# Kernel tuning notes

Hardware: AMD Instinct MI355X
Metric: run time of the kernel (lower is better)

Reference implementation:

```python
import jax, jax.numpy as jnp
import numpy as np

B = 16        # number of lists
N = 1024      # items per list (all equal)
D = 256       # feature dim (= dim_emb, need_embedding=False)


def setup_inputs() -> dict:
    key = jax.random.key(0)
    k1, k2, k3 = jax.random.split(key, 3)
    feats = jax.random.normal(k1, (B * N, D), dtype=jnp.float32)
    length = jnp.full((B,), N, dtype=jnp.int32)
    # Bilinear params: torch nn.Bilinear(d, d, 1) -> weight [1, d, d], bias [1]
    # xavier_uniform on the 3-d weight: bound = sqrt(6 / (fan_in + fan_out)) with
    # fan_in = d (last dim), fan_out = 1*d (per torch _calculate_fan_in_and_fan_out)
    bound = float(np.sqrt(6.0 / (D + D)))
    W_upper = jax.random.uniform(k2, (1, D, D), jnp.float32, -bound, bound)
    W_lower = jax.random.uniform(k3, (1, D, D), jnp.float32, -bound, bound)
    b_upper = jnp.zeros((1,), jnp.float32)
    b_lower = jnp.zeros((1,), jnp.float32)
    return {"feats": feats, "W_upper": W_upper, "b_upper": b_upper,
            "W_lower": W_lower, "b_lower": b_lower, "length": length}


def reference(feats, W_upper, b_upper, W_lower, b_lower, length):
    # nb_layers=0, need_embedding=False -> embedding and transformer are Identity.
    b = length.shape[0]
    n = feats.shape[0] // b  # equal-length lists -> static reshape
    d = feats.shape[-1]
    X = feats.reshape(b, n, d)  # [B, n, d]
    # For list i: repeated_feats_1 row (p*n + q) = x_p, repeated_feats_2 row = x_q,
    # so adjacency[p, q] = x_p^T W x_q + bias  (Bilinear with out=1).
    upper = jnp.einsum('bnd,de,bme->bnm', X, W_upper[0], X) + b_upper[0]
    lower = jnp.einsum('bnd,de,bme->bnm', X, W_lower[0], X) + b_lower[0]
    adj = jnp.triu(upper) + jnp.tril(lower, -1)  # [B, n, n]
    return adj
```

## Files before the change

kernel.cpp:

```cpp
#include <hip/hip_runtime.h>

#define BL 16
#define NL 1024
#define DD 256

typedef short bf16x8 __attribute__((ext_vector_type(8)));
typedef float f32x4 __attribute__((ext_vector_type(4)));

static __device__ __forceinline__ short f32_to_bf16(float f) {
  union { float f; unsigned u; } v; v.f = f;
  unsigned r = (v.u + 0x7FFFu + ((v.u >> 16) & 1u)) >> 16;
  return (short)r;
}

static __device__ __forceinline__ void g2l16(const short* g, short* l) {
  __builtin_amdgcn_global_load_lds(
      (const __attribute__((address_space(1))) void*)g,
      (__attribute__((address_space(3))) void*)l, 16, 0, 0);
}

__global__ __launch_bounds__(256) void k_prep(const float* __restrict__ X,
                                              const float* __restrict__ Wu,
                                              const float* __restrict__ Wl,
                                              short* __restrict__ Xb,
                                              short* __restrict__ WTu,
                                              short* __restrict__ WTl) {
  const int bid = blockIdx.x;
  if (bid < 4096) {
    int i = bid * 256 + threadIdx.x;
    const float4 v = ((const float4*)X)[i];
    short4 o;
    o.x = f32_to_bf16(v.x); o.y = f32_to_bf16(v.y);
    o.z = f32_to_bf16(v.z); o.w = f32_to_bf16(v.w);
    ((short4*)Xb)[i] = o;
  } else {
    const int id = bid - 4096;
    const int z = id >> 8, d = id & 255;
    const float* W = z ? Wl : Wu;
    short* WT = z ? WTl : WTu;
    const int e = threadIdx.x;
    WT[e * DD + d] = f32_to_bf16(W[d * DD + e]);
  }
}

static __device__ __forceinline__ void tile_pass(const short* __restrict__ Ylds,
                                                 const short* __restrict__ Bg,
                                                 float* __restrict__ Ob,
                                                 int p0, int q0, float bias,
                                                 int mode, int r, int quad) {
  f32x4 acc[4][4] = {};
#pragma unroll
  for (int ks = 0; ks < 8; ++ks) {
    bf16x8 af[4], bf[4];
#pragma unroll
    for (int mt = 0; mt < 4; ++mt) {
      const int row = mt * 16 + r;
      const int byte = (row * 512 + ks * 64 + quad * 16) ^ ((row & 7) << 4);
      af[mt] = *(const bf16x8*)((const char*)Ylds + byte);
    }
#pragma unroll
    for (int nt = 0; nt < 4; ++nt)
      bf[nt] = *(const bf16x8*)(Bg + (size_t)(nt * 16 + r) * DD + ks * 32 + quad * 8);
#pragma unroll
    for (int mt = 0; mt < 4; ++mt)
#pragma unroll
      for (int nt = 0; nt < 4; ++nt)
        acc[mt][nt] = __builtin_amdgcn_mfma_f32_16x16x32_bf16(af[mt], bf[nt],
                                                              acc[mt][nt], 0, 0, 0);
  }
#pragma unroll
  for (int mt = 0; mt < 4; ++mt)
#pragma unroll
    for (int nt = 0; nt < 4; ++nt) {
      const int q = q0 + nt * 16 + r;
#pragma unroll
      for (int i = 0; i < 4; ++i) {
        const int p = p0 + mt * 16 + quad * 4 + i;
        if (mode == 0 || (mode == 1 && q >= p) || (mode == 2 && q < p))
          Ob[(size_t)p * NL + q] = acc[mt][nt][i] + bias;
      }
    }
}

__global__ __launch_bounds__(512) void k_fused(const short* __restrict__ Xb,
                                               const short* __restrict__ WTu,
                                               const short* __restrict__ WTl,
                                               const float* __restrict__ bu_p,
                                               const float* __restrict__ bl_p,
                                               float* __restrict__ out) {
  __shared__ short Asw[64 * 256];
  __shared__ short Yu[64 * 256];
  __shared__ short Yl[64 * 256];

  const int bid = blockIdx.x;
  const int b = bid & 15, pt = bid >> 4;
  const int t = threadIdx.x, lane = t & 63, w = t >> 6;
  const int r = lane & 15, quad = lane >> 4;
  const size_t listoff = (size_t)b * NL * DD;
  const short* Ap = Xb + listoff + (size_t)pt * 64 * DD;

#pragma unroll
  for (int i = 0; i < 4; ++i) {
    const int c = i * 512 + t;
    const int src = (c & ~31) | ((c & 31) ^ ((c >> 5) & 7));
    g2l16(Ap + src * 8, Asw + c * 8);
  }
  __syncthreads();

  {
    const int n0 = w * 32;
    f32x4 aU[4][2] = {}, aL[4][2] = {};
#pragma unroll
    for (int ks = 0; ks < 8; ++ks) {
      bf16x8 af[4], bfu[2], bfl[2];
#pragma unroll
      for (int mt = 0; mt < 4; ++mt) {
        const int row = mt * 16 + r;
        const int byte = (row * 512 + ks * 64 + quad * 16) ^ ((row & 7) << 4);
        af[mt] = *(const bf16x8*)((const char*)Asw + byte);
      }
#pragma unroll
      for (int nt = 0; nt < 2; ++nt) {
        const int off = (n0 + nt * 16 + r) * DD + ks * 32 + quad * 8;
        bfu[nt] = *(const bf16x8*)(WTu + off);
        bfl[nt] = *(const bf16x8*)(WTl + off);
      }
#pragma unroll
      for (int mt = 0; mt < 4; ++mt)
#pragma unroll
        for (int nt = 0; nt < 2; ++nt) {
          aU[mt][nt] = __builtin_amdgcn_mfma_f32_16x16x32_bf16(af[mt], bfu[nt], aU[mt][nt], 0, 0, 0);
          aL[mt][nt] = __builtin_amdgcn_mfma_f32_16x16x32_bf16(af[mt], bfl[nt], aL[mt][nt], 0, 0, 0);
        }
    }
#pragma unroll
    for (int mt = 0; mt < 4; ++mt)
#pragma unroll
      for (int nt = 0; nt < 2; ++nt)
#pragma unroll
        for (int i = 0; i < 4; ++i) {
          const int row = mt * 16 + quad * 4 + i;
          const int col = n0 + nt * 16 + r;
          const int byte = (row * 512 + col * 2) ^ ((row & 7) << 4);
          *(short*)((char*)Yu + byte) = f32_to_bf16(aU[mt][nt][i]);
          *(short*)((char*)Yl + byte) = f32_to_bf16(aL[mt][nt][i]);
        }
  }
  __syncthreads();

  const float ubias = bu_p[0], lbias = bl_p[0];
  float* Ob = out + (size_t)b * NL * NL;
  const short* Bglist = Xb + listoff;
  const int p0 = pt * 64;

  for (int qq = 0; qq < 2; ++qq) {
    const int qt = w + qq * 8;
    const short* Bg = Bglist + (size_t)qt * 64 * DD;
    const int q0 = qt * 64;
    if (qt > pt) {
      tile_pass(Yu, Bg, Ob, p0, q0, ubias, 0, r, quad);
    } else if (qt < pt) {
      tile_pass(Yl, Bg, Ob, p0, q0, lbias, 0, r, quad);
    } else {
      tile_pass(Yu, Bg, Ob, p0, q0, ubias, 1, r, quad);
      tile_pass(Yl, Bg, Ob, p0, q0, lbias, 2, r, quad);
    }
  }
}

extern "C" void kernel_launch(void* const* d_in, const int* in_sizes, int n_in,
                              void* d_out, int out_size, void* d_ws, size_t ws_size,
                              hipStream_t stream) {
  const float* feats = (const float*)d_in[0];
  const float* Wu    = (const float*)d_in[1];
  const float* bu    = (const float*)d_in[2];
  const float* Wl    = (const float*)d_in[3];
  const float* bl    = (const float*)d_in[4];
  float* out = (float*)d_out;

  char* ws = (char*)d_ws;
  short* Xb  = (short*)(ws);
  short* WTu = (short*)(ws + (size_t)8 * 1024 * 1024);
  short* WTl = (short*)(ws + (size_t)8 * 1024 * 1024 + DD * DD * 2);

  k_prep<<<4096 + 512, 256, 0, stream>>>(feats, Wu, Wl, Xb, WTu, WTl);

  k_fused<<<256, 512, 0, stream>>>(Xb, WTu, WTl, bu, bl, out);
}
```

Baseline: 143.9 us.

## Halve row tile to 32, double grid, swap MFMA operands for vector stores

```diff
diff --git a/kernel.cpp b/kernel.cpp
--- a/kernel.cpp
+++ b/kernel.cpp
@@ -43,17 +43,17 @@
   }
 }
 
-static __device__ __forceinline__ void tile_pass(const short* __restrict__ Ylds,
-                                                 const short* __restrict__ Bg,
-                                                 float* __restrict__ Ob,
-                                                 int p0, int q0, float bias,
-                                                 int mode, int r, int quad) {
-  f32x4 acc[4][4] = {};
+static __device__ __forceinline__ void tile_off(const short* __restrict__ Ylds,
+                                                const short* __restrict__ Bg,
+                                                float* __restrict__ Ob,
+                                                int p0, int q0, float bias,
+                                                int r, int quad) {
+  f32x4 acc[4][2] = {};
 #pragma unroll
   for (int ks = 0; ks < 8; ++ks) {
-    bf16x8 af[4], bf[4];
-#pragma unroll
-    for (int mt = 0; mt < 4; ++mt) {
+    bf16x8 af[2], bf[4];
+#pragma unroll
+    for (int mt = 0; mt < 2; ++mt) {
       const int row = mt * 16 + r;
       const int byte = (row * 512 + ks * 64 + quad * 16) ^ ((row & 7) << 4);
       af[mt] = *(const bf16x8*)((const char*)Ylds + byte);
@@ -62,59 +62,102 @@
     for (int nt = 0; nt < 4; ++nt)
       bf[nt] = *(const bf16x8*)(Bg + (size_t)(nt * 16 + r) * DD + ks * 32 + quad * 8);
 #pragma unroll
-    for (int mt = 0; mt < 4; ++mt)
-#pragma unroll
-      for (int nt = 0; nt < 4; ++nt)
-        acc[mt][nt] = __builtin_amdgcn_mfma_f32_16x16x32_bf16(af[mt], bf[nt],
-                                                              acc[mt][nt], 0, 0, 0);
-  }
-#pragma unroll
-  for (int mt = 0; mt < 4; ++mt)
-#pragma unroll
-    for (int nt = 0; nt < 4; ++nt) {
-      const int q = q0 + nt * 16 + r;
+    for (int nt = 0; nt < 4; ++nt)
+#pragma unroll
+      for (int mt = 0; mt < 2; ++mt)
+        acc[nt][mt] = __builtin_amdgcn_mfma_f32_16x16x32_bf16(bf[nt], af[mt],
+                                                              acc[nt][mt], 0, 0, 0);
+  }
+#pragma unroll
+  for (int nt = 0; nt < 4; ++nt)
+#pragma unroll
+    for (int mt = 0; mt < 2; ++mt) {
+      const int p = p0 + mt * 16 + r;
+      const int q = q0 + nt * 16 + quad * 4;
+      f32x4 v;
+      v[0] = acc[nt][mt][0] + bias; v[1] = acc[nt][mt][1] + bias;
+      v[2] = acc[nt][mt][2] + bias; v[3] = acc[nt][mt][3] + bias;
+      __builtin_nontemporal_store(v, (f32x4*)(Ob + (size_t)p * NL + q));
+    }
+}
+
+static __device__ __forceinline__ void tile_diag(const short* __restrict__ Yu,
+                                                 const short* __restrict__ Yl,
+                                                 const short* __restrict__ Bg,
+                                                 float* __restrict__ Ob,
+                                                 int p0, int q0, float ub, float lb,
+                                                 int r, int quad) {
+  f32x4 aU[4][2] = {}, aL[4][2] = {};
+#pragma unroll
+  for (int ks = 0; ks < 8; ++ks) {
+    bf16x8 afu[2], afl[2], bf[4];
+#pragma unroll
+    for (int mt = 0; mt < 2; ++mt) {
+      const int row = mt * 16 + r;
+      const int byte = (row * 512 + ks * 64 + quad * 16) ^ ((row & 7) << 4);
+      afu[mt] = *(const bf16x8*)((const char*)Yu + byte);
+      afl[mt] = *(const bf16x8*)((const char*)Yl + byte);
+    }
+#pragma unroll
+    for (int nt = 0; nt < 4; ++nt)
+      bf[nt] = *(const bf16x8*)(Bg + (size_t)(nt * 16 + r) * DD + ks * 32 + quad * 8);
+#pragma unroll
+    for (int nt = 0; nt < 4; ++nt)
+#pragma unroll
+      for (int mt = 0; mt < 2; ++mt) {
+        aU[nt][mt] = __builtin_amdgcn_mfma_f32_16x16x32_bf16(bf[nt], afu[mt],
+                                                             aU[nt][mt], 0, 0, 0);
+        aL[nt][mt] = __builtin_amdgcn_mfma_f32_16x16x32_bf16(bf[nt], afl[mt],
+                                                             aL[nt][mt], 0, 0, 0);
+      }
+  }
+#pragma unroll
+  for (int nt = 0; nt < 4; ++nt)
+#pragma unroll
+    for (int mt = 0; mt < 2; ++mt) {
+      const int p = p0 + mt * 16 + r;
 #pragma unroll
       for (int i = 0; i < 4; ++i) {
-        const int p = p0 + mt * 16 + quad * 4 + i;
-        if (mode == 0 || (mode == 1 && q >= p) || (mode == 2 && q < p))
-          Ob[(size_t)p * NL + q] = acc[mt][nt][i] + bias;
-      }
-    }
-}
-
-__global__ __launch_bounds__(512) void k_fused(const short* __restrict__ Xb,
-                                               const short* __restrict__ WTu,
-                                               const short* __restrict__ WTl,
-                                               const float* __restrict__ bu_p,
-                                               const float* __restrict__ bl_p,
-                                               float* __restrict__ out) {
-  __shared__ short Asw[64 * 256];
-  __shared__ short Yu[64 * 256];
-  __shared__ short Yl[64 * 256];
+        const int q = q0 + nt * 16 + quad * 4 + i;
+        const float v = (q >= p) ? (aU[nt][mt][i] + ub) : (aL[nt][mt][i] + lb);
+        __builtin_nontemporal_store(v, Ob + (size_t)p * NL + q);
+      }
+    }
+}
+
+__global__ __launch_bounds__(512, 4) void k_fused(const short* __restrict__ Xb,
+                                                  const short* __restrict__ WTu,
+                                                  const short* __restrict__ WTl,
+                                                  const float* __restrict__ bu_p,
+                                                  const float* __restrict__ bl_p,
+                                                  float* __restrict__ out) {
+  __shared__ short Asw[32 * 256];
+  __shared__ short Yu[32 * 256];
+  __shared__ short Yl[32 * 256];
 
   const int bid = blockIdx.x;
   const int b = bid & 15, pt = bid >> 4;
   const int t = threadIdx.x, lane = t & 63, w = t >> 6;
   const int r = lane & 15, quad = lane >> 4;
   const size_t listoff = (size_t)b * NL * DD;
-  const short* Ap = Xb + listoff + (size_t)pt * 64 * DD;
-
-#pragma unroll
-  for (int i = 0; i < 4; ++i) {
+  const short* Ap = Xb + listoff + (size_t)pt * 32 * DD;
+
+#pragma unroll
+  for (int i = 0; i < 2; ++i) {
     const int c = i * 512 + t;
-    const int src = (c & ~31) | ((c & 31) ^ ((c >> 5) & 7));
+    const int src = c ^ ((c >> 5) & 7);
     g2l16(Ap + src * 8, Asw + c * 8);
   }
   __syncthreads();
 
   {
     const int n0 = w * 32;
-    f32x4 aU[4][2] = {}, aL[4][2] = {};
+    f32x4 aU[2][2] = {}, aL[2][2] = {};
 #pragma unroll
     for (int ks = 0; ks < 8; ++ks) {
-      bf16x8 af[4], bfu[2], bfl[2];
-#pragma unroll
-      for (int mt = 0; mt < 4; ++mt) {
+      bf16x8 af[2], bfu[2], bfl[2];
+#pragma unroll
+      for (int mt = 0; mt < 2; ++mt) {
         const int row = mt * 16 + r;
         const int byte = (row * 512 + ks * 64 + quad * 16) ^ ((row & 7) << 4);
         af[mt] = *(const bf16x8*)((const char*)Asw + byte);
@@ -126,7 +169,7 @@
         bfl[nt] = *(const bf16x8*)(WTl + off);
       }
 #pragma unroll
-      for (int mt = 0; mt < 4; ++mt)
+      for (int mt = 0; mt < 2; ++mt)
 #pragma unroll
         for (int nt = 0; nt < 2; ++nt) {
           aU[mt][nt] = __builtin_amdgcn_mfma_f32_16x16x32_bf16(af[mt], bfu[nt], aU[mt][nt], 0, 0, 0);
@@ -134,7 +177,7 @@
         }
     }
 #pragma unroll
-    for (int mt = 0; mt < 4; ++mt)
+    for (int mt = 0; mt < 2; ++mt)
 #pragma unroll
       for (int nt = 0; nt < 2; ++nt)
 #pragma unroll
@@ -148,22 +191,22 @@
   }
   __syncthreads();
 
-  const float ubias = bu_p[0], lbias = bl_p[0];
+  const float ub = bu_p[0], lb = bl_p[0];
   float* Ob = out + (size_t)b * NL * NL;
-  const short* Bglist = Xb + listoff;
-  const int p0 = pt * 64;
+  const short* Bl = Xb + listoff;
+  const int p0 = pt * 32;
+  const int dq = pt >> 1;
 
   for (int qq = 0; qq < 2; ++qq) {
     const int qt = w + qq * 8;
-    const short* Bg = Bglist + (size_t)qt * 64 * DD;
+    const short* Bg = Bl + (size_t)qt * 64 * DD;
     const int q0 = qt * 64;
-    if (qt > pt) {
-      tile_pass(Yu, Bg, Ob, p0, q0, ubias, 0, r, quad);
-    } else if (qt < pt) {
-      tile_pass(Yl, Bg, Ob, p0, q0, lbias, 0, r, quad);
+    if (qt > dq) {
+      tile_off(Yu, Bg, Ob, p0, q0, ub, r, quad);
+    } else if (qt < dq) {
+      tile_off(Yl, Bg, Ob, p0, q0, lb, r, quad);
     } else {
-      tile_pass(Yu, Bg, Ob, p0, q0, ubias, 1, r, quad);
-      tile_pass(Yl, Bg, Ob, p0, q0, lbias, 2, r, quad);
+      tile_diag(Yu, Yl, Bg, Ob, p0, q0, ub, lb, r, quad);
     }
   }
 }
@@ -185,5 +228,5 @@
 
   k_prep<<<4096 + 512, 256, 0, stream>>>(feats, Wu, Wl, Xb, WTu, WTl);
 
-  k_fused<<<256, 512, 0, stream>>>(Xb, WTu, WTl, bu, bl, out);
-}
+  k_fused<<<512, 512, 0, stream>>>(Xb, WTu, WTl, bu, bl, out);
+}
```

New measurement: 155.8 us. 8.3% more time.

## Use 1024-thread blocks with one q-tile per wave and vectorized stores

Applied to the files above, without the earlier changes.

```diff
diff --git a/kernel.cpp b/kernel.cpp
--- a/kernel.cpp
+++ b/kernel.cpp
@@ -43,51 +43,12 @@
   }
 }
 
-static __device__ __forceinline__ void tile_pass(const short* __restrict__ Ylds,
-                                                 const short* __restrict__ Bg,
-                                                 float* __restrict__ Ob,
-                                                 int p0, int q0, float bias,
-                                                 int mode, int r, int quad) {
-  f32x4 acc[4][4] = {};
-#pragma unroll
-  for (int ks = 0; ks < 8; ++ks) {
-    bf16x8 af[4], bf[4];
-#pragma unroll
-    for (int mt = 0; mt < 4; ++mt) {
-      const int row = mt * 16 + r;
-      const int byte = (row * 512 + ks * 64 + quad * 16) ^ ((row & 7) << 4);
-      af[mt] = *(const bf16x8*)((const char*)Ylds + byte);
-    }
-#pragma unroll
-    for (int nt = 0; nt < 4; ++nt)
-      bf[nt] = *(const bf16x8*)(Bg + (size_t)(nt * 16 + r) * DD + ks * 32 + quad * 8);
-#pragma unroll
-    for (int mt = 0; mt < 4; ++mt)
-#pragma unroll
-      for (int nt = 0; nt < 4; ++nt)
-        acc[mt][nt] = __builtin_amdgcn_mfma_f32_16x16x32_bf16(af[mt], bf[nt],
-                                                              acc[mt][nt], 0, 0, 0);
-  }
-#pragma unroll
-  for (int mt = 0; mt < 4; ++mt)
-#pragma unroll
-    for (int nt = 0; nt < 4; ++nt) {
-      const int q = q0 + nt * 16 + r;
-#pragma unroll
-      for (int i = 0; i < 4; ++i) {
-        const int p = p0 + mt * 16 + quad * 4 + i;
-        if (mode == 0 || (mode == 1 && q >= p) || (mode == 2 && q < p))
-          Ob[(size_t)p * NL + q] = acc[mt][nt][i] + bias;
-      }
-    }
-}
-
-__global__ __launch_bounds__(512) void k_fused(const short* __restrict__ Xb,
-                                               const short* __restrict__ WTu,
-                                               const short* __restrict__ WTl,
-                                               const float* __restrict__ bu_p,
-                                               const float* __restrict__ bl_p,
-                                               float* __restrict__ out) {
+__global__ __launch_bounds__(1024, 4) void k_fused(const short* __restrict__ Xb,
+                                                   const short* __restrict__ WTu,
+                                                   const short* __restrict__ WTl,
+                                                   const float* __restrict__ bu_p,
+                                                   const float* __restrict__ bl_p,
+                                                   float* __restrict__ out) {
   __shared__ short Asw[64 * 256];
   __shared__ short Yu[64 * 256];
   __shared__ short Yl[64 * 256];
@@ -100,70 +61,119 @@
   const short* Ap = Xb + listoff + (size_t)pt * 64 * DD;
 
 #pragma unroll
-  for (int i = 0; i < 4; ++i) {
-    const int c = i * 512 + t;
-    const int src = (c & ~31) | ((c & 31) ^ ((c >> 5) & 7));
+  for (int i = 0; i < 2; ++i) {
+    const int c = i * 1024 + t;
+    const int src = c ^ ((c >> 5) & 7);
     g2l16(Ap + src * 8, Asw + c * 8);
   }
   __syncthreads();
 
   {
-    const int n0 = w * 32;
-    f32x4 aU[4][2] = {}, aL[4][2] = {};
+    const int n0 = w * 16;
+    f32x4 aU[4] = {}, aL[4] = {};
 #pragma unroll
     for (int ks = 0; ks < 8; ++ks) {
-      bf16x8 af[4], bfu[2], bfl[2];
+      bf16x8 af[4];
 #pragma unroll
       for (int mt = 0; mt < 4; ++mt) {
         const int row = mt * 16 + r;
-        const int byte = (row * 512 + ks * 64 + quad * 16) ^ ((row & 7) << 4);
-        af[mt] = *(const bf16x8*)((const char*)Asw + byte);
+        const int abyte = (row * 512 + ks * 64 + quad * 16) ^ ((row & 7) << 4);
+        af[mt] = *(const bf16x8*)((const char*)Asw + abyte);
       }
+      const int off = (n0 + r) * DD + ks * 32 + quad * 8;
+      const bf16x8 bfu = *(const bf16x8*)(WTu + off);
+      const bf16x8 bfl = *(const bf16x8*)(WTl + off);
 #pragma unroll
-      for (int nt = 0; nt < 2; ++nt) {
-        const int off = (n0 + nt * 16 + r) * DD + ks * 32 + quad * 8;
-        bfu[nt] = *(const bf16x8*)(WTu + off);
-        bfl[nt] = *(const bf16x8*)(WTl + off);
+      for (int mt = 0; mt < 4; ++mt) {
+        aU[mt] = __builtin_amdgcn_mfma_f32_16x16x32_bf16(af[mt], bfu, aU[mt], 0, 0, 0);
+        aL[mt] = __builtin_amdgcn_mfma_f32_16x16x32_bf16(af[mt], bfl, aL[mt], 0, 0, 0);
       }
-#pragma unroll
-      for (int mt = 0; mt < 4; ++mt)
-#pragma unroll
-        for (int nt = 0; nt < 2; ++nt) {
-          aU[mt][nt] = __builtin_amdgcn_mfma_f32_16x16x32_bf16(af[mt], bfu[nt], aU[mt][nt], 0, 0, 0);
-          aL[mt][nt] = __builtin_amdgcn_mfma_f32_16x16x32_bf16(af[mt], bfl[nt], aL[mt][nt], 0, 0, 0);
-        }
     }
 #pragma unroll
     for (int mt = 0; mt < 4; ++mt)
 #pragma unroll
-      for (int nt = 0; nt < 2; ++nt)
-#pragma unroll
-        for (int i = 0; i < 4; ++i) {
-          const int row = mt * 16 + quad * 4 + i;
-          const int col = n0 + nt * 16 + r;
-          const int byte = (row * 512 + col * 2) ^ ((row & 7) << 4);
-          *(short*)((char*)Yu + byte) = f32_to_bf16(aU[mt][nt][i]);
-          *(short*)((char*)Yl + byte) = f32_to_bf16(aL[mt][nt][i]);
-        }
+      for (int i = 0; i < 4; ++i) {
+        const int row = mt * 16 + quad * 4 + i;
+        const int col = n0 + r;
+        const int byte = (row * 512 + col * 2) ^ ((row & 7) << 4);
+        *(short*)((char*)Yu + byte) = f32_to_bf16(aU[mt][i]);
+        *(short*)((char*)Yl + byte) = f32_to_bf16(aL[mt][i]);
+      }
   }
   __syncthreads();
 
-  const float ubias = bu_p[0], lbias = bl_p[0];
+  const float ub = bu_p[0], lb = bl_p[0];
   float* Ob = out + (size_t)b * NL * NL;
-  const short* Bglist = Xb + listoff;
   const int p0 = pt * 64;
+  const int qt = w, q0 = qt * 64;
+  const short* Bg = Xb + listoff + (size_t)qt * 64 * DD;
+  const short* YA = (qt >= pt) ? Yu : Yl;
+  const float bias = (qt >= pt) ? ub : lb;
 
-  for (int qq = 0; qq < 2; ++qq) {
-    const int qt = w + qq * 8;
-    const short* Bg = Bglist + (size_t)qt * 64 * DD;
-    const int q0 = qt * 64;
-    if (qt > pt) {
-      tile_pass(Yu, Bg, Ob, p0, q0, ubias, 0, r, quad);
-    } else if (qt < pt) {
-      tile_pass(Yl, Bg, Ob, p0, q0, lbias, 0, r, quad);
-    } else {
-      tile_pass(Yu, Bg, Ob, p0, q0, ubias, 1, r, quad);
-      tile_pass(Yl, Bg, Ob, p0, q0, lbias, 2, r, quad);
+  f32x4 acc[4][4] = {};
+#pragma unroll
+  for (int ks = 0; ks < 8; ++ks) {
+    bf16x8 af[4], bf[4];
+#pragma unroll
+    for (int mt = 0; mt < 4; ++mt) {
+      const int row = mt * 16 + r;
+      const int abyte = (row * 512 + ks * 64 + quad * 16) ^ ((row & 7) << 4);
+      af[mt] = *(const bf16x8*)((const char*)YA + abyte);
+    }
+#pragma unroll
+    for (int nt = 0; nt < 4; ++nt)
+      bf[nt] = *(const bf16x8*)(Bg + (size_t)(nt * 16 + r) * DD + ks * 32 + quad * 8);
+#pragma unroll
+    for (int nt = 0; nt < 4; ++nt)
+#pragma unroll
+      for (int mt = 0; mt < 4; ++mt)
+        acc[nt][mt] = __builtin_amdgcn_mfma_f32_16x16x32_bf16(bf[nt], af[mt],
+                                                              acc[nt][mt], 0, 0, 0);
+  }
+#pragma unroll
+  for (int mt = 0; mt < 4; ++mt) {
+    float* row = Ob + (size_t)(p0 + mt * 16 + r) * NL;
+#pragma unroll
+    for (int nt = 0; nt < 4; ++nt) {
+      f32x4 v;
+#pragma unroll
+      for (int i = 0; i < 4; ++i) v[i] = acc[nt][mt][i] + bias;
+      *(f32x4*)(row + q0 + nt * 16 + quad * 4) = v;
+    }
+  }
+
+  if (qt == pt) {
+    f32x4 accL[4][4] = {};
+#pragma unroll
+    for (int ks = 0; ks < 8; ++ks) {
+      bf16x8 af[4], bf[4];
+#pragma unroll
+      for (int mt = 0; mt < 4; ++mt) {
+        const int row = mt * 16 + r;
+        const int abyte = (row * 512 + ks * 64 + quad * 16) ^ ((row & 7) << 4);
+        af[mt] = *(const bf16x8*)((const char*)Yl + abyte);
+      }
+#pragma unroll
+      for (int nt = 0; nt < 4; ++nt)
+        bf[nt] = *(const bf16x8*)(Bg + (size_t)(nt * 16 + r) * DD + ks * 32 + quad * 8);
+#pragma unroll
+      for (int nt = 0; nt < 4; ++nt)
+#pragma unroll
+        for (int mt = 0; mt < 4; ++mt)
+          accL[nt][mt] = __builtin_amdgcn_mfma_f32_16x16x32_bf16(bf[nt], af[mt],
+                                                                 accL[nt][mt], 0, 0, 0);
+    }
+#pragma unroll
+    for (int mt = 0; mt < 4; ++mt) {
+      const int p = p0 + mt * 16 + r;
+      float* row = Ob + (size_t)p * NL;
+#pragma unroll
+      for (int nt = 0; nt < 4; ++nt)
+#pragma unroll
+        for (int i = 0; i < 4; ++i) {
+          const int q = q0 + nt * 16 + quad * 4 + i;
+          if (q < p) row[q] = accL[nt][mt][i] + lb;
+        }
     }
   }
 }
@@ -185,5 +195,5 @@
 
   k_prep<<<4096 + 512, 256, 0, stream>>>(feats, Wu, Wl, Xb, WTu, WTl);
 
-  k_fused<<<256, 512, 0, stream>>>(Xb, WTu, WTl, bu, bl, out);
+  k_fused<<<256, 1024, 0, stream>>>(Xb, WTu, WTl, bu, bl, out);
 }
```

New measurement: 130.5 us. 1.1x faster.
